# Kernel tuning notes

Measured on AMD Instinct MI355X. Metric: run time of the kernel, lower is better.

## Reference

```python
import jax, jax.numpy as jnp
import numpy as np

DIM = 512        # model dim
MOE_DIM = 256    # expert hidden dim
E = 64           # n_routed experts
G = 8            # n_routed_group
TOPK_G = 4       # n_topk_group
K = 8            # n_experts_per_tok
SCALE = 2.5      # routed_scale
CAP = 1024


def setup_inputs() -> dict:
    key = jax.random.key(0)
    ks = jax.random.split(key, 6)
    x = jax.random.normal(ks[0], (4, 512, DIM), jnp.float32)
    gate_w = jax.random.normal(ks[1], (E, DIM), jnp.float32) / np.sqrt(DIM).astype(np.float32)
    gate_b = jax.random.normal(ks[2], (E,), jnp.float32) * 0.01
    w1 = jax.random.normal(ks[3], (E, DIM, MOE_DIM), jnp.float32) / np.sqrt(DIM).astype(np.float32)
    w3 = jax.random.normal(ks[4], (E, DIM, MOE_DIM), jnp.float32) / np.sqrt(DIM).astype(np.float32)
    w2 = jax.random.normal(ks[5], (E, MOE_DIM, DIM), jnp.float32) / np.sqrt(MOE_DIM).astype(np.float32)
    return {"x": x, "gate_w": gate_w, "gate_b": gate_b, "w1": w1, "w3": w3, "w2": w2}


def _gate(x2, gate_w, gate_b):
    # x2: [T, DIM] -> (weights [T,K], indices [T,K])
    T = x2.shape[0]
    scores = jax.nn.sigmoid(x2 @ gate_w.T)                      # [T, E]
    s = (scores + gate_b).reshape(T, G, E // G)                  # grouped scores
    group_scores = jax.lax.top_k(s, 2)[0].sum(-1)                # [T, G] sum of top-2 per group
    top_groups = jax.lax.top_k(group_scores, TOPK_G)[1]          # [T, TOPK_G]
    gmask = jnp.zeros((T, G), bool).at[jnp.arange(T)[:, None], top_groups].set(True)
    s = jnp.where(gmask[..., None], s, -jnp.inf).reshape(T, E)
    idx = jax.lax.top_k(s, K)[1]                                 # [T, K]
    w = jnp.take_along_axis(scores, idx, axis=1)                 # original (pre-bias) scores
    w = w / w.sum(-1, keepdims=True) * SCALE
    return w, idx


def _moe_forward(x, gate_w, gate_b, w1, w3, w2):
    shape = x.shape
    x2 = x.reshape(-1, DIM)                                      # [T, DIM]
    T = x2.shape[0]
    w, idx = _gate(x2, gate_w, gate_b)
    flat_e = idx.reshape(-1)                                     # [T*K]
    # position of each (token, slot) within its expert's buffer, in order
    oh = (flat_e[:, None] == jnp.arange(E)[None, :]).astype(jnp.int32)  # [T*K, E]
    pos = (jnp.cumsum(oh, axis=0) * oh).sum(-1) - 1              # [T*K]
    x_rep = jnp.repeat(x2, K, axis=0)                            # [T*K, DIM]
    # dispatch into per-expert buffers [E, CAP, DIM]
    xb = jnp.zeros((E, CAP, DIM), x2.dtype).at[flat_e, pos].set(x_rep, mode='drop')
    h = jax.nn.silu(jnp.einsum('ecd,edm->ecm', xb, w1)) * jnp.einsum('ecd,edm->ecm', xb, w3)
    yb = jnp.einsum('ecm,emd->ecd', h, w2)                       # [E, CAP, DIM]
    # combine: gather back and weight
    y = yb.at[flat_e, pos].get(mode='fill', fill_value=0.0) * w.reshape(-1)[:, None]
    return y.reshape(T, K, DIM).sum(1).reshape(shape)


def reference(x, gate_w, gate_b, w1, w3, w2):
    return _moe_forward(x, gate_w, gate_b, w1, w3, w2)
```

## Files before the change

### kernel.cpp

```cpp
#include <hip/hip_runtime.h>

#define T_TOK 2048
#define DIM   512
#define MOE   256
#define NE    64
#define NG    8
#define TOPKG 4
#define TOPK  8
#define CAP   1024
#define MOE_SCALE 2.5f

typedef float f32x4 __attribute__((ext_vector_type(4)));
typedef short s16x8 __attribute__((ext_vector_type(8)));

__device__ __forceinline__ unsigned short f2bf(float f) {
    unsigned u = __builtin_bit_cast(unsigned, f);
    unsigned r = (u + 0x7fffu + ((u >> 16) & 1u)) >> 16;
    return (unsigned short)r;
}
__device__ __forceinline__ unsigned pk2(float lo, float hi) {
    return (unsigned)f2bf(lo) | ((unsigned)f2bf(hi) << 16);
}

__global__ __launch_bounds__(256) void gwt_k(const float* __restrict__ gw,
                                             float* __restrict__ gwT)
{
    int idx = blockIdx.x * 256 + threadIdx.x;
    int e = idx >> 9, k = idx & 511;
    gwT[(size_t)(k >> 2) * 256 + e * 4 + (k & 3)] = gw[idx];
}

__global__ __launch_bounds__(256) void gate_fused_k(const float* __restrict__ x,
                                                    const float* __restrict__ gwT,
                                                    const float* __restrict__ gb,
                                                    int* __restrict__ counts,
                                                    int* __restrict__ etok,
                                                    float* __restrict__ wt_of,
                                                    short* __restrict__ xb)
{
    __shared__ float xs[4][512];
    __shared__ float ps[4][4][64];
    int w = threadIdx.x >> 6, lane = threadIdx.x & 63;
    int t = blockIdx.x * 4 + w;

    {
        const float4* xr = (const float4*)(x + (size_t)t * DIM);
        float4 v0 = xr[lane * 2], v1 = xr[lane * 2 + 1];
        *(float4*)&xs[w][lane * 8]     = v0;
        *(float4*)&xs[w][lane * 8 + 4] = v1;
        short o[8];
        o[0] = (short)f2bf(v0.x); o[1] = (short)f2bf(v0.y);
        o[2] = (short)f2bf(v0.z); o[3] = (short)f2bf(v0.w);
        o[4] = (short)f2bf(v1.x); o[5] = (short)f2bf(v1.y);
        o[6] = (short)f2bf(v1.z); o[7] = (short)f2bf(v1.w);
        *(s16x8*)(xb + (size_t)t * DIM + lane * 8) = *(const s16x8*)o;
    }
    __syncthreads();

    const f32x4* gt = (const f32x4*)gwT;
    float a0 = 0.f, a1 = 0.f, a2 = 0.f, a3 = 0.f;
    int kb = w * 32;
#pragma unroll 8
    for (int k4 = 0; k4 < 32; ++k4) {
        f32x4 g  = gt[(size_t)(kb + k4) * 64 + lane];
        f32x4 x0 = *(const f32x4*)&xs[0][(kb + k4) * 4];
        f32x4 x1 = *(const f32x4*)&xs[1][(kb + k4) * 4];
        f32x4 x2 = *(const f32x4*)&xs[2][(kb + k4) * 4];
        f32x4 x3 = *(const f32x4*)&xs[3][(kb + k4) * 4];
        a0 += g.x * x0.x + g.y * x0.y + g.z * x0.z + g.w * x0.w;
        a1 += g.x * x1.x + g.y * x1.y + g.z * x1.z + g.w * x1.w;
        a2 += g.x * x2.x + g.y * x2.y + g.z * x2.z + g.w * x2.w;
        a3 += g.x * x3.x + g.y * x3.y + g.z * x3.z + g.w * x3.w;
    }
    ps[w][0][lane] = a0; ps[w][1][lane] = a1;
    ps[w][2][lane] = a2; ps[w][3][lane] = a3;
    __syncthreads();
    float acc = ps[0][w][lane] + ps[1][w][lane] + ps[2][w][lane] + ps[3][w][lane];

    float sc = 1.f / (1.f + __expf(-acc));
    float s  = sc + gb[lane];

    float m1 = s, m2 = -1e30f;
#pragma unroll
    for (int d = 1; d < 8; d <<= 1) {
        float o1 = __shfl_xor(m1, d);
        float o2 = __shfl_xor(m2, d);
        float n1 = fmaxf(m1, o1);
        float n2 = fmaxf(fminf(m1, o1), fmaxf(m2, o2));
        m1 = n1; m2 = n2;
    }
    float gv = m1 + m2;

    bool gkeep = false;
#pragma unroll
    for (int it = 0; it < TOPKG; ++it) {
        float m = gv;
#pragma unroll
        for (int d = 1; d < 64; d <<= 1) m = fmaxf(m, __shfl_xor(m, d));
        unsigned long long mask = __ballot(gv == m);
        int ldr = __ffsll(mask) - 1;
        if ((lane >> 3) == (ldr >> 3)) { gkeep = true; gv = -2e30f; }
    }
    float sv = gkeep ? s : -1e30f;

    float wsum = 0.f;
    int my_e = 0; float my_w = 0.f;
#pragma unroll
    for (int k = 0; k < TOPK; ++k) {
        float m = sv;
#pragma unroll
        for (int d = 1; d < 64; d <<= 1) m = fmaxf(m, __shfl_xor(m, d));
        unsigned long long mask = __ballot(sv == m);
        int l = __ffsll(mask) - 1;
        float wk = __shfl(sc, l);
        wsum += wk;
        if (lane == k) { my_e = l; my_w = wk; }
        if (lane == l) sv = -2e30f;
    }
    float scale = MOE_SCALE / wsum;
    if (lane < TOPK) {
        int p = atomicAdd(&counts[my_e], 1);
        int rid = t * TOPK + lane;
        bool ok = (p < CAP);
        if (ok) etok[my_e * CAP + p] = rid;
        wt_of[rid] = ok ? my_w * scale : 0.f;
    }
}

__global__ __launch_bounds__(64) void scan_k(const int* __restrict__ counts,
                                             int* __restrict__ tbase)
{
    int lane = threadIdx.x;
    int ne = min(counts[lane], CAP);
    int nt = (ne + 31) >> 5;
    int v = nt;
#pragma unroll
    for (int d = 1; d < 64; d <<= 1) {
        int o = __shfl_up(v, d);
        if (lane >= d) v += o;
    }
    tbase[lane] = v - nt;
}

__global__ __launch_bounds__(256, 2) void gemm1_k(const short* __restrict__ xb,
                                                  const float* __restrict__ w1,
                                                  const float* __restrict__ w3,
                                                  const int* __restrict__ counts,
                                                  const int* __restrict__ etok,
                                                  const int* __restrict__ tbase,
                                                  short* __restrict__ hgf)
{
    __shared__ short Bl[2][16][2][64][8];
    __shared__ short Ct[4][2][16][24];

    int e  = blockIdx.x & 63, cg = blockIdx.x >> 6;
    int n0 = cg * 32;
    int tid = threadIdx.x;
    int w = tid >> 6, lane = tid & 63;
    int q = lane >> 4, m16 = lane & 15;

    const float* W1e = w1 + (size_t)e * DIM * MOE + n0;
    const float* W3e = w3 + (size_t)e * DIM * MOE + n0;
#pragma unroll 4
    for (int it = 0; it < 16; ++it) {
        int idx = it * 256 + tid;
        int mat = idx >> 11;
        int rem = idx & 2047;
        int r2  = rem >> 3;
        int cq  = (rem & 7) * 4;
        int k   = r2 * 2;
        int kt = k >> 5, qf = (k >> 3) & 3, j0 = k & 7;
        int cgrp = cq >> 4, c15 = cq & 15;
        const float* p = (mat ? W3e : W1e) + (size_t)k * MOE + cq;
        f32x4 lo = __builtin_nontemporal_load((const f32x4*)p);
        f32x4 hi = __builtin_nontemporal_load((const f32x4*)(p + MOE));
        unsigned* b = (unsigned*)&Bl[mat][kt][cgrp][qf * 16 + c15][j0];
        b[0]  = pk2(lo.x, hi.x);
        b[4]  = pk2(lo.y, hi.y);
        b[8]  = pk2(lo.z, hi.z);
        b[12] = pk2(lo.w, hi.w);
    }
    __syncthreads();

    int ne = min(counts[e], CAP);
    int nt = (ne + 31) >> 5;
    int G0 = tbase[e];
    const int* el = etok + e * CAP;

    int row0 = w * 32 + m16, row1 = row0 + 16;
    int tr0 = 0, tr1 = 0;
    if (w < nt) {
        tr0 = el[row0 < ne ? row0 : ne - 1];
        tr1 = el[row1 < ne ? row1 : ne - 1];
    }

    for (int T = w; T < nt; T += 4) {
        const short* A0 = xb + (size_t)(tr0 >> 3) * DIM + q * 8;
        const short* A1 = xb + (size_t)(tr1 >> 3) * DIM + q * 8;
        if (T + 4 < nt) {
            int nr0 = (T + 4) * 32 + m16, nr1 = nr0 + 16;
            tr0 = el[nr0 < ne ? nr0 : ne - 1];
            tr1 = el[nr1 < ne ? nr1 : ne - 1];
        }

        f32x4 acc[2][2][2];
#pragma unroll
        for (int i = 0; i < 2; ++i)
#pragma unroll
            for (int j = 0; j < 2; ++j)
#pragma unroll
                for (int c = 0; c < 2; ++c) acc[i][j][c] = (f32x4)0.f;

        s16x8 pa0[4], pa1[4];
#pragma unroll
        for (int i = 0; i < 4; ++i) {
            pa0[i] = *(const s16x8*)(A0 + i * 32);
            pa1[i] = *(const s16x8*)(A1 + i * 32);
        }
#pragma unroll
        for (int kt = 0; kt < 16; ++kt) {
            s16x8 a0 = pa0[kt & 3], a1 = pa1[kt & 3];
            if (kt < 12) {
                pa0[kt & 3] = *(const s16x8*)(A0 + (kt + 4) * 32);
                pa1[kt & 3] = *(const s16x8*)(A1 + (kt + 4) * 32);
            }
            s16x8 b10 = *(const s16x8*)&Bl[0][kt][0][lane][0];
            s16x8 b11 = *(const s16x8*)&Bl[0][kt][1][lane][0];
            s16x8 b30 = *(const s16x8*)&Bl[1][kt][0][lane][0];
            s16x8 b31 = *(const s16x8*)&Bl[1][kt][1][lane][0];
            acc[0][0][0] = __builtin_amdgcn_mfma_f32_16x16x32_bf16(a0, b10, acc[0][0][0], 0, 0, 0);
            acc[1][0][0] = __builtin_amdgcn_mfma_f32_16x16x32_bf16(a1, b10, acc[1][0][0], 0, 0, 0);
            acc[0][0][1] = __builtin_amdgcn_mfma_f32_16x16x32_bf16(a0, b11, acc[0][0][1], 0, 0, 0);
            acc[1][0][1] = __builtin_amdgcn_mfma_f32_16x16x32_bf16(a1, b11, acc[1][0][1], 0, 0, 0);
            acc[0][1][0] = __builtin_amdgcn_mfma_f32_16x16x32_bf16(a0, b30, acc[0][1][0], 0, 0, 0);
            acc[1][1][0] = __builtin_amdgcn_mfma_f32_16x16x32_bf16(a1, b30, acc[1][1][0], 0, 0, 0);
            acc[0][1][1] = __builtin_amdgcn_mfma_f32_16x16x32_bf16(a0, b31, acc[0][1][1], 0, 0, 0);
            acc[1][1][1] = __builtin_amdgcn_mfma_f32_16x16x32_bf16(a1, b31, acc[1][1][1], 0, 0, 0);
        }

#pragma unroll
        for (int cgrp = 0; cgrp < 2; ++cgrp) {
#pragma unroll
            for (int sub = 0; sub < 2; ++sub)
#pragma unroll
                for (int r = 0; r < 4; ++r) {
                    float g = acc[sub][0][cgrp][r];
                    float u = acc[sub][1][cgrp][r];
                    float hv = g / (1.f + __expf(-g)) * u;
                    Ct[w][sub][q * 4 + r][m16] = (short)f2bf(hv);
                }
            int subr = q >> 1;
            s16x8 hv8 = *(const s16x8*)&Ct[w][subr][m16][(q & 1) * 8];
            size_t slot = ((size_t)(G0 + T) * 8 + cg) * 2 + subr;
            *(s16x8*)(hgf + slot * 512 + (cgrp * 2 + (q & 1)) * 128 + m16 * 8) = hv8;
        }
    }
}

__global__ __launch_bounds__(256, 2) void gemm2_k(const short* __restrict__ hgf,
                                                  const float* __restrict__ w2,
                                                  const int* __restrict__ counts,
                                                  const int* __restrict__ etok,
                                                  const int* __restrict__ tbase,
                                                  short* __restrict__ ybuf)
{
    __shared__ short Bl[4][8][64][8];

    int e  = blockIdx.x & 63, cg = blockIdx.x >> 6;
    int n0 = cg * 64;
    int tid = threadIdx.x;
    int w = tid >> 6, lane = tid & 63;
    int q = lane >> 4, m16 = lane & 15;

    const float* W2e = w2 + (size_t)e * MOE * DIM + n0;
#pragma unroll 4
    for (int it = 0; it < 8; ++it) {
        int idx = it * 256 + tid;
        int r2  = idx >> 4;
        int cq  = (idx & 15) * 4;
        int k   = r2 * 2;
        int kt2 = k >> 5, qf = (k >> 3) & 3, j0 = k & 7;
        int s = cq >> 4, c15 = cq & 15;
        const float* p = W2e + (size_t)k * DIM + cq;
        f32x4 lo = __builtin_nontemporal_load((const f32x4*)p);
        f32x4 hi = __builtin_nontemporal_load((const f32x4*)(p + DIM));
        unsigned* b = (unsigned*)&Bl[s][kt2][qf * 16 + c15][j0];
        b[0]  = pk2(lo.x, hi.x);
        b[4]  = pk2(lo.y, hi.y);
        b[8]  = pk2(lo.z, hi.z);
        b[12] = pk2(lo.w, hi.w);
    }
    __syncthreads();

    int ne = min(counts[e], CAP);
    int nt = (ne + 31) >> 5;
    int G0 = tbase[e];
    const int* el = etok + e * CAP;

    for (int T = w; T < nt; T += 4) {
        const short* A = hgf + (size_t)(G0 + T) * 8192 + lane * 8;

        int erid[2][4];
#pragma unroll
        for (int sub = 0; sub < 2; ++sub)
#pragma unroll
            for (int r = 0; r < 4; ++r) {
                int row = T * 32 + sub * 16 + q * 4 + r;
                erid[sub][r] = row < ne ? el[row] : -1;
            }

        f32x4 acc[2][4];
#pragma unroll
        for (int i = 0; i < 2; ++i)
#pragma unroll
            for (int j = 0; j < 4; ++j) acc[i][j] = (f32x4)0.f;

        s16x8 pa0[4], pa1[4];
#pragma unroll
        for (int i = 0; i < 4; ++i) {
            pa0[i] = *(const s16x8*)(A + (i * 2 + 0) * 512);
            pa1[i] = *(const s16x8*)(A + (i * 2 + 1) * 512);
        }
#pragma unroll
        for (int kt = 0; kt < 8; ++kt) {
            s16x8 a0 = pa0[kt & 3], a1 = pa1[kt & 3];
            if (kt < 4) {
                pa0[kt & 3] = *(const s16x8*)(A + ((kt + 4) * 2 + 0) * 512);
                pa1[kt & 3] = *(const s16x8*)(A + ((kt + 4) * 2 + 1) * 512);
            }
            s16x8 b0 = *(const s16x8*)&Bl[0][kt][lane][0];
            s16x8 b1 = *(const s16x8*)&Bl[1][kt][lane][0];
            s16x8 b2 = *(const s16x8*)&Bl[2][kt][lane][0];
            s16x8 b3 = *(const s16x8*)&Bl[3][kt][lane][0];
            acc[0][0] = __builtin_amdgcn_mfma_f32_16x16x32_bf16(a0, b0, acc[0][0], 0, 0, 0);
            acc[1][0] = __builtin_amdgcn_mfma_f32_16x16x32_bf16(a1, b0, acc[1][0], 0, 0, 0);
            acc[0][1] = __builtin_amdgcn_mfma_f32_16x16x32_bf16(a0, b1, acc[0][1], 0, 0, 0);
            acc[1][1] = __builtin_amdgcn_mfma_f32_16x16x32_bf16(a1, b1, acc[1][1], 0, 0, 0);
            acc[0][2] = __builtin_amdgcn_mfma_f32_16x16x32_bf16(a0, b2, acc[0][2], 0, 0, 0);
            acc[1][2] = __builtin_amdgcn_mfma_f32_16x16x32_bf16(a1, b2, acc[1][2], 0, 0, 0);
            acc[0][3] = __builtin_amdgcn_mfma_f32_16x16x32_bf16(a0, b3, acc[0][3], 0, 0, 0);
            acc[1][3] = __builtin_amdgcn_mfma_f32_16x16x32_bf16(a1, b3, acc[1][3], 0, 0, 0);
        }

#pragma unroll
        for (int sub = 0; sub < 2; ++sub)
#pragma unroll
            for (int s = 0; s < 4; ++s)
#pragma unroll
                for (int r = 0; r < 4; ++r) {
                    if (erid[sub][r] >= 0)
                        ybuf[(size_t)erid[sub][r] * DIM + n0 + s * 16 + m16] =
                            (short)f2bf(acc[sub][s][r]);
                }
    }
}

__global__ __launch_bounds__(256) void combine_k(const short* __restrict__ ybuf,
                                                 const float* __restrict__ wt_of,
                                                 float* __restrict__ out)
{
    int t = blockIdx.x;
    int tid = threadIdx.x;
    const int* yb = (const int*)ybuf;
    float sx = 0.f, sy = 0.f;
#pragma unroll
    for (int k = 0; k < TOPK; ++k) {
        float wk = wt_of[t * TOPK + k];
        int v = yb[(size_t)(t * TOPK + k) * (DIM / 2) + tid];
        float lo = __builtin_bit_cast(float, (unsigned)v << 16);
        float hi = __builtin_bit_cast(float, (unsigned)v & 0xffff0000u);
        sx += wk * lo;
        sy += wk * hi;
    }
    float2 o = {sx, sy};
    ((float2*)out)[(size_t)t * (DIM / 2) + tid] = o;
}

extern "C" void kernel_launch(void* const* d_in, const int* in_sizes, int n_in,
                              void* d_out, int out_size, void* d_ws, size_t ws_size,
                              hipStream_t stream)
{
    const float* x  = (const float*)d_in[0];
    const float* gw = (const float*)d_in[1];
    const float* gb = (const float*)d_in[2];
    const float* w1 = (const float*)d_in[3];
    const float* w3 = (const float*)d_in[4];
    const float* w2 = (const float*)d_in[5];

    char* ws = (char*)d_ws;
    short* xb    = (short*)(ws);
    short* hgf   = (short*)(ws + 2097152);
    short* ybuf  = (short*)(ws + 11534336);
    float* gwT   = (float*)(ws + 28311552);
    int*   etok  = (int*)  (ws + 28442624);
    float* wt_of = (float*)(ws + 28704768);
    int*   counts= (int*)  (ws + 28770304);
    int*   tbase = (int*)  (ws + 28770560);

    hipMemsetAsync(counts, 0, NE * 4, stream);

    gwt_k<<<128, 256, 0, stream>>>(gw, gwT);
    gate_fused_k<<<T_TOK / 4, 256, 0, stream>>>(x, gwT, gb, counts, etok, wt_of, xb);
    scan_k<<<1, 64, 0, stream>>>(counts, tbase);
    gemm1_k<<<NE * 8, 256, 0, stream>>>(xb, w1, w3, counts, etok, tbase, hgf);
    gemm2_k<<<NE * 8, 256, 0, stream>>>(hgf, w2, counts, etok, tbase, ybuf);
    combine_k<<<T_TOK, 256, 0, stream>>>(ybuf, wt_of, (float*)d_out);
}
```

Before: 240.6 us.

## Fuse combine into gemm2 via atomics and inline expert tile scan

Removes the scan kernel by having each gemm block compute the per-expert tile prefix sum with wave shuffles, and removes the combine kernel by having gemm2 scale its outputs by routing weights and atomically add them into a zeroed fp32 output. The bf16 intermediate buffer round trip and two launches go away, at the cost of an extra memset of the output and many fp32 atomics with contention across the eight experts per token. It also deepens the A-operand prefetch in gemm1, loads all A fragments up front in gemm2, and switches weight loads from nontemporal to normal loads. Results become order-nondeterministic in their fp32 summation.

```diff
diff --git a/kernel.cpp b/kernel.cpp
--- a/kernel.cpp
+++ b/kernel.cpp
@@ -20,6 +20,22 @@
 }
 __device__ __forceinline__ unsigned pk2(float lo, float hi) {
     return (unsigned)f2bf(lo) | ((unsigned)f2bf(hi) << 16);
+}
+
+__device__ __forceinline__ void tile_scan(const int* __restrict__ counts, int lane,
+                                          int e, int& G0, int& ne, int& nt)
+{
+    int cl = min(counts[lane], CAP);
+    int ntl = (cl + 31) >> 5;
+    int v = ntl;
+#pragma unroll
+    for (int d = 1; d < 64; d <<= 1) {
+        int o = __shfl_up(v, d);
+        if (lane >= d) v += o;
+    }
+    G0 = __shfl(v - ntl, e);
+    ne = __shfl(cl, e);
+    nt = __shfl(ntl, e);
 }
 
 __global__ __launch_bounds__(256) void gwt_k(const float* __restrict__ gw,
@@ -127,27 +143,11 @@
     }
 }
 
-__global__ __launch_bounds__(64) void scan_k(const int* __restrict__ counts,
-                                             int* __restrict__ tbase)
-{
-    int lane = threadIdx.x;
-    int ne = min(counts[lane], CAP);
-    int nt = (ne + 31) >> 5;
-    int v = nt;
-#pragma unroll
-    for (int d = 1; d < 64; d <<= 1) {
-        int o = __shfl_up(v, d);
-        if (lane >= d) v += o;
-    }
-    tbase[lane] = v - nt;
-}
-
 __global__ __launch_bounds__(256, 2) void gemm1_k(const short* __restrict__ xb,
                                                   const float* __restrict__ w1,
                                                   const float* __restrict__ w3,
                                                   const int* __restrict__ counts,
                                                   const int* __restrict__ etok,
-                                                  const int* __restrict__ tbase,
                                                   short* __restrict__ hgf)
 {
     __shared__ short Bl[2][16][2][64][8];
@@ -158,6 +158,9 @@
     int tid = threadIdx.x;
     int w = tid >> 6, lane = tid & 63;
     int q = lane >> 4, m16 = lane & 15;
+
+    int G0, ne, nt;
+    tile_scan(counts, lane, e, G0, ne, nt);
 
     const float* W1e = w1 + (size_t)e * DIM * MOE + n0;
     const float* W3e = w3 + (size_t)e * DIM * MOE + n0;
@@ -172,8 +175,8 @@
         int kt = k >> 5, qf = (k >> 3) & 3, j0 = k & 7;
         int cgrp = cq >> 4, c15 = cq & 15;
         const float* p = (mat ? W3e : W1e) + (size_t)k * MOE + cq;
-        f32x4 lo = __builtin_nontemporal_load((const f32x4*)p);
-        f32x4 hi = __builtin_nontemporal_load((const f32x4*)(p + MOE));
+        f32x4 lo = *(const f32x4*)p;
+        f32x4 hi = *(const f32x4*)(p + MOE);
         unsigned* b = (unsigned*)&Bl[mat][kt][cgrp][qf * 16 + c15][j0];
         b[0]  = pk2(lo.x, hi.x);
         b[4]  = pk2(lo.y, hi.y);
@@ -182,9 +185,6 @@
     }
     __syncthreads();
 
-    int ne = min(counts[e], CAP);
-    int nt = (ne + 31) >> 5;
-    int G0 = tbase[e];
     const int* el = etok + e * CAP;
 
     int row0 = w * 32 + m16, row1 = row0 + 16;
@@ -211,18 +211,18 @@
 #pragma unroll
                 for (int c = 0; c < 2; ++c) acc[i][j][c] = (f32x4)0.f;
 
-        s16x8 pa0[4], pa1[4];
-#pragma unroll
-        for (int i = 0; i < 4; ++i) {
+        s16x8 pa0[8], pa1[8];
+#pragma unroll
+        for (int i = 0; i < 8; ++i) {
             pa0[i] = *(const s16x8*)(A0 + i * 32);
             pa1[i] = *(const s16x8*)(A1 + i * 32);
         }
 #pragma unroll
         for (int kt = 0; kt < 16; ++kt) {
-            s16x8 a0 = pa0[kt & 3], a1 = pa1[kt & 3];
-            if (kt < 12) {
-                pa0[kt & 3] = *(const s16x8*)(A0 + (kt + 4) * 32);
-                pa1[kt & 3] = *(const s16x8*)(A1 + (kt + 4) * 32);
+            s16x8 a0 = pa0[kt & 7], a1 = pa1[kt & 7];
+            if (kt < 8) {
+                pa0[kt & 7] = *(const s16x8*)(A0 + (kt + 8) * 32);
+                pa1[kt & 7] = *(const s16x8*)(A1 + (kt + 8) * 32);
             }
             s16x8 b10 = *(const s16x8*)&Bl[0][kt][0][lane][0];
             s16x8 b11 = *(const s16x8*)&Bl[0][kt][1][lane][0];
@@ -261,8 +261,8 @@
                                                   const float* __restrict__ w2,
                                                   const int* __restrict__ counts,
                                                   const int* __restrict__ etok,
-                                                  const int* __restrict__ tbase,
-                                                  short* __restrict__ ybuf)
+                                                  const float* __restrict__ wt_of,
+                                                  float* __restrict__ out)
 {
     __shared__ short Bl[4][8][64][8];
 
@@ -271,6 +271,9 @@
     int tid = threadIdx.x;
     int w = tid >> 6, lane = tid & 63;
     int q = lane >> 4, m16 = lane & 15;
+
+    int G0, ne, nt;
+    tile_scan(counts, lane, e, G0, ne, nt);
 
     const float* W2e = w2 + (size_t)e * MOE * DIM + n0;
 #pragma unroll 4
@@ -282,8 +285,8 @@
         int kt2 = k >> 5, qf = (k >> 3) & 3, j0 = k & 7;
         int s = cq >> 4, c15 = cq & 15;
         const float* p = W2e + (size_t)k * DIM + cq;
-        f32x4 lo = __builtin_nontemporal_load((const f32x4*)p);
-        f32x4 hi = __builtin_nontemporal_load((const f32x4*)(p + DIM));
+        f32x4 lo = *(const f32x4*)p;
+        f32x4 hi = *(const f32x4*)(p + DIM);
         unsigned* b = (unsigned*)&Bl[s][kt2][qf * 16 + c15][j0];
         b[0]  = pk2(lo.x, hi.x);
         b[4]  = pk2(lo.y, hi.y);
@@ -292,42 +295,37 @@
     }
     __syncthreads();
 
-    int ne = min(counts[e], CAP);
-    int nt = (ne + 31) >> 5;
-    int G0 = tbase[e];
     const int* el = etok + e * CAP;
 
     for (int T = w; T < nt; T += 4) {
         const short* A = hgf + (size_t)(G0 + T) * 8192 + lane * 8;
 
-        int erid[2][4];
+        int   erid[2][4];
+        float wtr[2][4];
 #pragma unroll
         for (int sub = 0; sub < 2; ++sub)
 #pragma unroll
             for (int r = 0; r < 4; ++r) {
                 int row = T * 32 + sub * 16 + q * 4 + r;
-                erid[sub][r] = row < ne ? el[row] : -1;
+                int rid = row < ne ? el[row] : -1;
+                erid[sub][r] = rid;
+                wtr[sub][r]  = rid >= 0 ? wt_of[rid] : 0.f;
             }
 
+        s16x8 pa[16];
+#pragma unroll
+        for (int i = 0; i < 16; ++i)
+            pa[i] = *(const s16x8*)(A + i * 512);
+
         f32x4 acc[2][4];
 #pragma unroll
         for (int i = 0; i < 2; ++i)
 #pragma unroll
             for (int j = 0; j < 4; ++j) acc[i][j] = (f32x4)0.f;
 
-        s16x8 pa0[4], pa1[4];
-#pragma unroll
-        for (int i = 0; i < 4; ++i) {
-            pa0[i] = *(const s16x8*)(A + (i * 2 + 0) * 512);
-            pa1[i] = *(const s16x8*)(A + (i * 2 + 1) * 512);
-        }
 #pragma unroll
         for (int kt = 0; kt < 8; ++kt) {
-            s16x8 a0 = pa0[kt & 3], a1 = pa1[kt & 3];
-            if (kt < 4) {
-                pa0[kt & 3] = *(const s16x8*)(A + ((kt + 4) * 2 + 0) * 512);
-                pa1[kt & 3] = *(const s16x8*)(A + ((kt + 4) * 2 + 1) * 512);
-            }
+            s16x8 a0 = pa[kt * 2], a1 = pa[kt * 2 + 1];
             s16x8 b0 = *(const s16x8*)&Bl[0][kt][lane][0];
             s16x8 b1 = *(const s16x8*)&Bl[1][kt][lane][0];
             s16x8 b2 = *(const s16x8*)&Bl[2][kt][lane][0];
@@ -345,35 +343,17 @@
 #pragma unroll
         for (int sub = 0; sub < 2; ++sub)
 #pragma unroll
-            for (int s = 0; s < 4; ++s)
-#pragma unroll
-                for (int r = 0; r < 4; ++r) {
-                    if (erid[sub][r] >= 0)
-                        ybuf[(size_t)erid[sub][r] * DIM + n0 + s * 16 + m16] =
-                            (short)f2bf(acc[sub][s][r]);
+            for (int r = 0; r < 4; ++r) {
+                int rid = erid[sub][r];
+                if (rid >= 0) {
+                    float* op = out + (size_t)(rid >> 3) * DIM + n0 + m16;
+                    float wk = wtr[sub][r];
+#pragma unroll
+                    for (int s = 0; s < 4; ++s)
+                        atomicAdd(op + s * 16, wk * acc[sub][s][r]);
                 }
-    }
-}
-
-__global__ __launch_bounds__(256) void combine_k(const short* __restrict__ ybuf,
-                                                 const float* __restrict__ wt_of,
-                                                 float* __restrict__ out)
-{
-    int t = blockIdx.x;
-    int tid = threadIdx.x;
-    const int* yb = (const int*)ybuf;
-    float sx = 0.f, sy = 0.f;
-#pragma unroll
-    for (int k = 0; k < TOPK; ++k) {
-        float wk = wt_of[t * TOPK + k];
-        int v = yb[(size_t)(t * TOPK + k) * (DIM / 2) + tid];
-        float lo = __builtin_bit_cast(float, (unsigned)v << 16);
-        float hi = __builtin_bit_cast(float, (unsigned)v & 0xffff0000u);
-        sx += wk * lo;
-        sy += wk * hi;
-    }
-    float2 o = {sx, sy};
-    ((float2*)out)[(size_t)t * (DIM / 2) + tid] = o;
+            }
+    }
 }
 
 extern "C" void kernel_launch(void* const* d_in, const int* in_sizes, int n_in,
@@ -390,19 +370,16 @@
     char* ws = (char*)d_ws;
     short* xb    = (short*)(ws);
     short* hgf   = (short*)(ws + 2097152);
-    short* ybuf  = (short*)(ws + 11534336);
     float* gwT   = (float*)(ws + 28311552);
     int*   etok  = (int*)  (ws + 28442624);
     float* wt_of = (float*)(ws + 28704768);
     int*   counts= (int*)  (ws + 28770304);
-    int*   tbase = (int*)  (ws + 28770560);
 
     hipMemsetAsync(counts, 0, NE * 4, stream);
+    hipMemsetAsync(d_out, 0, (size_t)T_TOK * DIM * 4, stream);
 
     gwt_k<<<128, 256, 0, stream>>>(gw, gwT);
     gate_fused_k<<<T_TOK / 4, 256, 0, stream>>>(x, gwT, gb, counts, etok, wt_of, xb);
-    scan_k<<<1, 64, 0, stream>>>(counts, tbase);
-    gemm1_k<<<NE * 8, 256, 0, stream>>>(xb, w1, w3, counts, etok, tbase, hgf);
-    gemm2_k<<<NE * 8, 256, 0, stream>>>(hgf, w2, counts, etok, tbase, ybuf);
-    combine_k<<<T_TOK, 256, 0, stream>>>(ybuf, wt_of, (float*)d_out);
-}
+    gemm1_k<<<NE * 8, 256, 0, stream>>>(xb, w1, w3, counts, etok, hgf);
+    gemm2_k<<<NE * 8, 256, 0, stream>>>(hgf, w2, counts, etok, wt_of, (float*)d_out);
+}
```

Result: slower. 270.1 us (+12.3%).

## Pre-gather tokens into MFMA-ready per-tile layout and fold scan into kernels

Applied to the files above, without the earlier changes.

Adds a dispatch kernel that gathers each expert's routed token rows from xb into a contiguous, MFMA-fragment-ordered buffer, so gemm1 reads its A operand with contiguous loads instead of indirect per-row gathers through etok. The separate scan kernel is removed; each kernel recomputes the per-expert tile prefix sum with a wave shuffle scan. This trades an extra pass over the dispatched activations (and a new launch) for simpler, coalesced A loads in gemm1 and one fewer tiny launch. xg aliases ybuf's workspace region, which relies on gemm1 finishing before gemm2 writes ybuf.

```diff
diff --git a/kernel.cpp b/kernel.cpp
--- a/kernel.cpp
+++ b/kernel.cpp
@@ -20,6 +20,22 @@
 }
 __device__ __forceinline__ unsigned pk2(float lo, float hi) {
     return (unsigned)f2bf(lo) | ((unsigned)f2bf(hi) << 16);
+}
+
+__device__ __forceinline__ void tile_scan(const int* __restrict__ counts, int lane,
+                                          int e, int& G0, int& ne, int& nt)
+{
+    int cl = min(counts[lane], CAP);
+    int ntl = (cl + 31) >> 5;
+    int v = ntl;
+#pragma unroll
+    for (int d = 1; d < 64; d <<= 1) {
+        int o = __shfl_up(v, d);
+        if (lane >= d) v += o;
+    }
+    G0 = __shfl(v - ntl, e);
+    ne = __shfl(cl, e);
+    nt = __shfl(ntl, e);
 }
 
 __global__ __launch_bounds__(256) void gwt_k(const float* __restrict__ gw,
@@ -127,27 +143,37 @@
     }
 }
 
-__global__ __launch_bounds__(64) void scan_k(const int* __restrict__ counts,
-                                             int* __restrict__ tbase)
-{
-    int lane = threadIdx.x;
-    int ne = min(counts[lane], CAP);
-    int nt = (ne + 31) >> 5;
-    int v = nt;
-#pragma unroll
-    for (int d = 1; d < 64; d <<= 1) {
-        int o = __shfl_up(v, d);
-        if (lane >= d) v += o;
-    }
-    tbase[lane] = v - nt;
-}
-
-__global__ __launch_bounds__(256, 2) void gemm1_k(const short* __restrict__ xb,
+__global__ __launch_bounds__(256) void dispatch_k(const short* __restrict__ xb,
+                                                  const int* __restrict__ counts,
+                                                  const int* __restrict__ etok,
+                                                  short* __restrict__ xg)
+{
+    int e = blockIdx.x & 63, sub = blockIdx.x >> 6;
+    int w = threadIdx.x >> 6, lane = threadIdx.x & 63;
+
+    int G0, ne, nt;
+    tile_scan(counts, lane, e, G0, ne, nt);
+    int rows = nt * 32;
+    const int* el = etok + e * CAP;
+
+    int kt = lane >> 2, qq = lane & 3;
+    for (int p = sub * 4 + w; p < rows; p += 32) {
+        s16x8 v = {0, 0, 0, 0, 0, 0, 0, 0};
+        if (p < ne) {
+            int tok = el[p] >> 3;
+            v = *(const s16x8*)(xb + (size_t)tok * DIM + lane * 8);
+        }
+        int st = (p >> 4) & 1, m = p & 15;
+        size_t off = ((((size_t)(G0 + (p >> 5)) * 16 + kt) * 2 + st) * 64
+                      + (qq * 16 + m)) * 8;
+        *(s16x8*)(xg + off) = v;
+    }
+}
+
+__global__ __launch_bounds__(256, 2) void gemm1_k(const short* __restrict__ xg,
                                                   const float* __restrict__ w1,
                                                   const float* __restrict__ w3,
                                                   const int* __restrict__ counts,
-                                                  const int* __restrict__ etok,
-                                                  const int* __restrict__ tbase,
                                                   short* __restrict__ hgf)
 {
     __shared__ short Bl[2][16][2][64][8];
@@ -158,6 +184,9 @@
     int tid = threadIdx.x;
     int w = tid >> 6, lane = tid & 63;
     int q = lane >> 4, m16 = lane & 15;
+
+    int G0, ne, nt;
+    tile_scan(counts, lane, e, G0, ne, nt);
 
     const float* W1e = w1 + (size_t)e * DIM * MOE + n0;
     const float* W3e = w3 + (size_t)e * DIM * MOE + n0;
@@ -182,26 +211,8 @@
     }
     __syncthreads();
 
-    int ne = min(counts[e], CAP);
-    int nt = (ne + 31) >> 5;
-    int G0 = tbase[e];
-    const int* el = etok + e * CAP;
-
-    int row0 = w * 32 + m16, row1 = row0 + 16;
-    int tr0 = 0, tr1 = 0;
-    if (w < nt) {
-        tr0 = el[row0 < ne ? row0 : ne - 1];
-        tr1 = el[row1 < ne ? row1 : ne - 1];
-    }
-
     for (int T = w; T < nt; T += 4) {
-        const short* A0 = xb + (size_t)(tr0 >> 3) * DIM + q * 8;
-        const short* A1 = xb + (size_t)(tr1 >> 3) * DIM + q * 8;
-        if (T + 4 < nt) {
-            int nr0 = (T + 4) * 32 + m16, nr1 = nr0 + 16;
-            tr0 = el[nr0 < ne ? nr0 : ne - 1];
-            tr1 = el[nr1 < ne ? nr1 : ne - 1];
-        }
+        const short* A = xg + (size_t)(G0 + T) * 16384 + lane * 8;
 
         f32x4 acc[2][2][2];
 #pragma unroll
@@ -214,15 +225,15 @@
         s16x8 pa0[4], pa1[4];
 #pragma unroll
         for (int i = 0; i < 4; ++i) {
-            pa0[i] = *(const s16x8*)(A0 + i * 32);
-            pa1[i] = *(const s16x8*)(A1 + i * 32);
+            pa0[i] = *(const s16x8*)(A + (i * 2 + 0) * 512);
+            pa1[i] = *(const s16x8*)(A + (i * 2 + 1) * 512);
         }
 #pragma unroll
         for (int kt = 0; kt < 16; ++kt) {
             s16x8 a0 = pa0[kt & 3], a1 = pa1[kt & 3];
             if (kt < 12) {
-                pa0[kt & 3] = *(const s16x8*)(A0 + (kt + 4) * 32);
-                pa1[kt & 3] = *(const s16x8*)(A1 + (kt + 4) * 32);
+                pa0[kt & 3] = *(const s16x8*)(A + ((kt + 4) * 2 + 0) * 512);
+                pa1[kt & 3] = *(const s16x8*)(A + ((kt + 4) * 2 + 1) * 512);
             }
             s16x8 b10 = *(const s16x8*)&Bl[0][kt][0][lane][0];
             s16x8 b11 = *(const s16x8*)&Bl[0][kt][1][lane][0];
@@ -261,7 +272,6 @@
                                                   const float* __restrict__ w2,
                                                   const int* __restrict__ counts,
                                                   const int* __restrict__ etok,
-                                                  const int* __restrict__ tbase,
                                                   short* __restrict__ ybuf)
 {
     __shared__ short Bl[4][8][64][8];
@@ -271,6 +281,9 @@
     int tid = threadIdx.x;
     int w = tid >> 6, lane = tid & 63;
     int q = lane >> 4, m16 = lane & 15;
+
+    int G0, ne, nt;
+    tile_scan(counts, lane, e, G0, ne, nt);
 
     const float* W2e = w2 + (size_t)e * MOE * DIM + n0;
 #pragma unroll 4
@@ -292,9 +305,6 @@
     }
     __syncthreads();
 
-    int ne = min(counts[e], CAP);
-    int nt = (ne + 31) >> 5;
-    int G0 = tbase[e];
     const int* el = etok + e * CAP;
 
     for (int T = w; T < nt; T += 4) {
@@ -390,19 +400,19 @@
     char* ws = (char*)d_ws;
     short* xb    = (short*)(ws);
     short* hgf   = (short*)(ws + 2097152);
+    short* xg    = (short*)(ws + 11534336);
     short* ybuf  = (short*)(ws + 11534336);
-    float* gwT   = (float*)(ws + 28311552);
-    int*   etok  = (int*)  (ws + 28442624);
-    float* wt_of = (float*)(ws + 28704768);
-    int*   counts= (int*)  (ws + 28770304);
-    int*   tbase = (int*)  (ws + 28770560);
+    float* gwT   = (float*)(ws + 30408704);
+    int*   etok  = (int*)  (ws + 30539776);
+    float* wt_of = (float*)(ws + 30801920);
+    int*   counts= (int*)  (ws + 30867456);
 
     hipMemsetAsync(counts, 0, NE * 4, stream);
 
     gwt_k<<<128, 256, 0, stream>>>(gw, gwT);
     gate_fused_k<<<T_TOK / 4, 256, 0, stream>>>(x, gwT, gb, counts, etok, wt_of, xb);
-    scan_k<<<1, 64, 0, stream>>>(counts, tbase);
-    gemm1_k<<<NE * 8, 256, 0, stream>>>(xb, w1, w3, counts, etok, tbase, hgf);
-    gemm2_k<<<NE * 8, 256, 0, stream>>>(hgf, w2, counts, etok, tbase, ybuf);
+    dispatch_k<<<NE * 8, 256, 0, stream>>>(xb, counts, etok, xg);
+    gemm1_k<<<NE * 8, 256, 0, stream>>>(xg, w1, w3, counts, hgf);
+    gemm2_k<<<NE * 8, 256, 0, stream>>>(hgf, w2, counts, etok, ybuf);
     combine_k<<<T_TOK, 256, 0, stream>>>(ybuf, wt_of, (float*)d_out);
 }
```

Result: slower. 246.8 us (+2.6%).
